# Optimization experiments

Measured on AMD Instinct MI355X. Metric: run time of the kernel, lower is better.

The kernel has to match this reference:

```python
import jax, jax.numpy as jnp
import numpy as np

N_SITES, NODE_F = 50000, 64
N_PERM, N_NEIGH = 12, 8
IN_F = N_NEIGH * NODE_F  # 512
OUT_F = 64
LN2 = float(np.log(2.0))


def setup_inputs() -> dict:
    key = jax.random.key(0)
    k1, k2, k3, k4 = jax.random.split(key, 4)
    X_sites = jax.random.normal(k1, (N_SITES, NODE_F), dtype=jnp.float32)
    X_NSs = jax.random.randint(k2, (N_SITES, N_PERM, N_NEIGH), 0, N_SITES)
    # nn.Linear(IN_F, OUT_F): weight (OUT_F, IN_F), bias (OUT_F,)
    bound = 1.0 / np.sqrt(IN_F)
    W = jax.random.uniform(k3, (OUT_F, IN_F), minval=-bound, maxval=bound, dtype=jnp.float32)
    b = jax.random.uniform(k4, (OUT_F,), minval=-bound, maxval=bound, dtype=jnp.float32)
    return {"X_sites": X_sites, "X_NSs": X_NSs, "W": W, "b": b}


def reference(X_sites, X_NSs, W, b):
    # Gather neighbor features: (N, P, K, F) -> (N, P, K*F)
    gathered = X_sites[X_NSs].reshape(X_NSs.shape[0], N_PERM, IN_F)
    # Linear: (N, P, IN_F) @ (IN_F, OUT_F) + b
    x1 = jnp.einsum('npi,oi->npo', gathered, W) + b
    # Shifted softplus: softplus(x) - log(2)  (dropout treated as identity / eval mode)
    x2 = jax.nn.softplus(x1) - LN2
    # Sum over permutations -> (N, OUT_F)
    return x2.sum(axis=1)
```

## Files before the change

kernel.cpp:

```cpp
#include <hip/hip_runtime.h>
#include <hip/hip_bf16.h>

#define N_SITES 50000
#define N_PERM  12
#define N_NEIGH 8
#define NODE_F  64
#define IN_F    512
#define OUT_F   64
#define N_TILES (N_SITES / 16)
#define LN2F    0.69314718055994530942f

#define XCHUNKS (N_SITES * NODE_F / 8)
#define WCHUNKS (OUT_F * IN_F / 8)
#define SLOT_E  520
#define BUF_E   (16 * SLOT_E)

typedef __bf16 bf16x8 __attribute__((ext_vector_type(8)));
typedef float  f32x4  __attribute__((ext_vector_type(4)));

__device__ __forceinline__ unsigned short f32_to_bf16_rne(unsigned int u) {
    u += 0x7FFFu + ((u >> 16) & 1u);
    return (unsigned short)(u >> 16);
}

__device__ __forceinline__ int probe_is_bf16(const void* Xorig) {
    int lane = threadIdx.x & 63;
    unsigned short h = ((const unsigned short*)Xorig)[2 * lane];
    int e = (h >> 7) & 0xFF;
    unsigned long long mm = __ballot(e >= 110 && e <= 140);
    return (__popcll(mm) >= 48) ? 1 : 0;
}

__device__ __forceinline__ void pack8(const uint4* src, uint4* dst, int c) {
    uint4 a = src[2 * c], b = src[2 * c + 1];
    uint4 o;
    o.x = (unsigned int)f32_to_bf16_rne(a.x) | ((unsigned int)f32_to_bf16_rne(a.y) << 16);
    o.y = (unsigned int)f32_to_bf16_rne(a.z) | ((unsigned int)f32_to_bf16_rne(a.w) << 16);
    o.z = (unsigned int)f32_to_bf16_rne(b.x) | ((unsigned int)f32_to_bf16_rne(b.y) << 16);
    o.w = (unsigned int)f32_to_bf16_rne(b.z) | ((unsigned int)f32_to_bf16_rne(b.w) << 16);
    dst[c] = o;
}

__global__ void convert_all(const void* __restrict__ Xv, const void* __restrict__ Wv,
                            const void* __restrict__ Bv, uint4* __restrict__ Xb,
                            uint4* __restrict__ Wb, float* __restrict__ Bf) {
    const int isbf = probe_is_bf16(Xv);
    int c = blockIdx.x * blockDim.x + threadIdx.x;
    if (c < XCHUNKS) {
        if (isbf) Xb[c] = ((const uint4*)Xv)[c];
        else      pack8((const uint4*)Xv, Xb, c);
    } else if (c < XCHUNKS + WCHUNKS) {
        int cw = c - XCHUNKS;
        if (isbf) Wb[cw] = ((const uint4*)Wv)[cw];
        else      pack8((const uint4*)Wv, Wb, cw);
    } else if (c < XCHUNKS + WCHUNKS + OUT_F) {
        int i = c - XCHUNKS - WCHUNKS;
        Bf[i] = isbf ? (float)((const __bf16*)Bv)[i] : ((const float*)Bv)[i];
    }
}

__device__ __forceinline__ float softplus_sh(float x) {
    float t = __expf(-fabsf(x));
    return fmaxf(x, 0.f) + 0.69314718056f * __log2f(1.f + t);
}

__device__ __forceinline__ void async16(const __bf16* g, __bf16* l) {
    __builtin_amdgcn_global_load_lds(
        (const __attribute__((address_space(1))) unsigned int*)g,
        (__attribute__((address_space(3))) unsigned int*)l, 16, 0, 0);
}

__global__ __launch_bounds__(256, 2)
void lcnn_dma(const void* __restrict__ Xorig, const __bf16* __restrict__ Xb,
              const int* __restrict__ NS, const __bf16* __restrict__ Wb,
              const float* __restrict__ Bf, void* __restrict__ outv)
{
    __shared__ __align__(16) __bf16 Abuf[2][BUF_E];

    const int wave = threadIdx.x >> 6;
    const int lane = threadIdx.x & 63;
    const int m    = lane & 15;
    const int quad = lane >> 4;
    const int mk   = m & 7;
    const int mh   = m >> 3;
    const int tile = blockIdx.x;

    bf16x8 Wfrag[16];
    #pragma unroll
    for (int ks = 0; ks < 16; ++ks)
        Wfrag[ks] = *(const bf16x8*)(Wb + (size_t)(wave * 16 + m) * IN_F + ks * 32 + quad * 8);

    const float bias = Bf[wave * 16 + m];

    auto load_idx = [&](int p_, int out[4]) {
        #pragma unroll
        for (int i = 0; i < 4; ++i) {
            int t = wave * 4 + i;
            int s = ((t & 1) << 3) + (lane >> 3);
            int k = t >> 1;
            out[i] = NS[(size_t)(tile * 16 + s) * (N_PERM * N_NEIGH) + p_ * N_NEIGH + k];
        }
    };
    auto stage = [&](int buf_, const int idxv[4]) {
        const int csrc = (lane & 7) ^ (lane >> 3);
        #pragma unroll
        for (int i = 0; i < 4; ++i) {
            int t = wave * 4 + i;
            async16(Xb + (size_t)idxv[i] * NODE_F + csrc * 8, &Abuf[buf_][t * SLOT_E]);
        }
    };

    int idxn[4];
    load_idx(0, idxn);
    stage(0, idxn);
    load_idx(1, idxn);
    __syncthreads();

    f32x4 sum = {0.f, 0.f, 0.f, 0.f};
    for (int p = 0; p < N_PERM; ++p) {
        if (p < N_PERM - 1) stage((p + 1) & 1, idxn);
        if (p < N_PERM - 2) load_idx(p + 2, idxn);

        f32x4 acc = {0.f, 0.f, 0.f, 0.f};
        const __bf16* bb = &Abuf[p & 1][0];
        #pragma unroll
        for (int ks = 0; ks < 16; ++ks) {
            int t_r = (ks >> 1) * 2 + mh;
            int j   = ((ks & 1) << 2) | quad;
            bf16x8 afr = *(const bf16x8*)(bb + t_r * SLOT_E + mk * 64 + ((j ^ mk) << 3));
            acc = __builtin_amdgcn_mfma_f32_16x16x32_bf16(afr, Wfrag[ks], acc, 0, 0, 0);
        }
        #pragma unroll
        for (int r = 0; r < 4; ++r) sum[r] += softplus_sh(acc[r] + bias);
        __syncthreads();
    }

    const int isbf = probe_is_bf16(Xorig);
    #pragma unroll
    for (int r = 0; r < 4; ++r) {
        size_t pos = (size_t)(tile * 16 + quad * 4 + r) * OUT_F + wave * 16 + m;
        float v = sum[r] - 12.0f * LN2F;
        if (isbf) ((__bf16*)outv)[pos] = (__bf16)v;
        else      ((float*)outv)[pos]  = v;
    }
}

__global__ void lcnn_fallback(const float* __restrict__ X, const int* __restrict__ NS,
                              const float* __restrict__ W, const float* __restrict__ B,
                              float* __restrict__ out) {
    int t = blockIdx.x * blockDim.x + threadIdx.x;
    if (t >= N_SITES * OUT_F) return;
    int sitei = t >> 6, o = t & 63;
    const int* ns = NS + (size_t)sitei * 96;
    float s = 0.f;
    for (int p = 0; p < N_PERM; ++p) {
        float x = B[o];
        for (int n = 0; n < N_NEIGH; ++n) {
            const float* xr = X + (size_t)ns[p * 8 + n] * NODE_F;
            const float* wr = W + (size_t)o * IN_F + n * NODE_F;
            for (int f = 0; f < NODE_F; ++f) x += xr[f] * wr[f];
        }
        s += softplus_sh(x);
    }
    out[t] = s - 12.0f * LN2F;
}

extern "C" void kernel_launch(void* const* d_in, const int* in_sizes, int n_in,
                              void* d_out, int out_size, void* d_ws, size_t ws_size,
                              hipStream_t stream) {
    const void* X  = d_in[0];
    const int*  NS = (const int*)d_in[1];
    const void* W  = d_in[2];
    const void* B  = d_in[3];

    char* ws = (char*)d_ws;
    __bf16* Xb = (__bf16*)ws;
    __bf16* Wb = (__bf16*)(ws + (size_t)XCHUNKS * 16);
    float*  Bf = (float*)(ws + (size_t)(XCHUNKS + WCHUNKS) * 16);
    const bool conv = ws_size >= (size_t)(XCHUNKS + WCHUNKS) * 16 + OUT_F * 4;

    if (conv) {
        int nch = XCHUNKS + WCHUNKS + OUT_F;
        hipLaunchKernelGGL(convert_all, dim3((nch + 255) / 256), dim3(256), 0, stream,
                           X, W, B, (uint4*)Xb, (uint4*)Wb, Bf);
        hipLaunchKernelGGL(lcnn_dma, dim3(N_TILES), dim3(256), 0, stream,
                           X, Xb, NS, Wb, Bf, d_out);
    } else {
        hipLaunchKernelGGL(lcnn_fallback,
                           dim3((N_SITES * OUT_F + 255) / 256), dim3(256), 0, stream,
                           (const float*)X, NS, (const float*)W, (const float*)B,
                           (float*)d_out);
    }
}
```

Measured before the change: 146.1 us.

## Use two waves per block with each wave computing two 16-column output fragments

Blocks shrink from four waves to two. Each wave now holds W fragments for 32 output columns and issues two MFMAs per A fragment read from LDS. This halves LDS A-fragment reads per MFMA and doubles each wave's share of gather staging. In exchange it doubles W register usage, to 128 VGPRs for the fragments, and each wave issues twice as many async gathers, which could hurt latency hiding or occupancy.

```diff
diff --git a/kernel.cpp b/kernel.cpp
--- a/kernel.cpp
+++ b/kernel.cpp
@@ -70,14 +70,14 @@
         (__attribute__((address_space(3))) unsigned int*)l, 16, 0, 0);
 }
 
-__global__ __launch_bounds__(256, 2)
+__global__ __launch_bounds__(128, 2)
 void lcnn_dma(const void* __restrict__ Xorig, const __bf16* __restrict__ Xb,
               const int* __restrict__ NS, const __bf16* __restrict__ Wb,
               const float* __restrict__ Bf, void* __restrict__ outv)
 {
     __shared__ __align__(16) __bf16 Abuf[2][BUF_E];
 
-    const int wave = threadIdx.x >> 6;
+    const int wn   = threadIdx.x >> 6;
     const int lane = threadIdx.x & 63;
     const int m    = lane & 15;
     const int quad = lane >> 4;
@@ -85,63 +85,80 @@
     const int mh   = m >> 3;
     const int tile = blockIdx.x;
 
-    bf16x8 Wfrag[16];
+    bf16x8 Wfrag[16][2];
     #pragma unroll
-    for (int ks = 0; ks < 16; ++ks)
-        Wfrag[ks] = *(const bf16x8*)(Wb + (size_t)(wave * 16 + m) * IN_F + ks * 32 + quad * 8);
-
-    const float bias = Bf[wave * 16 + m];
-
-    auto load_idx = [&](int p_, int out[4]) {
-        #pragma unroll
-        for (int i = 0; i < 4; ++i) {
-            int t = wave * 4 + i;
+    for (int ks = 0; ks < 16; ++ks) {
+        #pragma unroll
+        for (int nf = 0; nf < 2; ++nf)
+            Wfrag[ks][nf] = *(const bf16x8*)(Wb + (size_t)(wn * 32 + nf * 16 + m) * IN_F
+                                             + ks * 32 + quad * 8);
+    }
+
+    const float bias0 = Bf[wn * 32 + m];
+    const float bias1 = Bf[wn * 32 + 16 + m];
+
+    auto load_idx = [&](int p_, int out[8]) {
+        #pragma unroll
+        for (int i = 0; i < 8; ++i) {
+            int t = wn * 8 + i;
             int s = ((t & 1) << 3) + (lane >> 3);
             int k = t >> 1;
             out[i] = NS[(size_t)(tile * 16 + s) * (N_PERM * N_NEIGH) + p_ * N_NEIGH + k];
         }
     };
-    auto stage = [&](int buf_, const int idxv[4]) {
+    auto stage = [&](int buf_, const int idxv[8]) {
         const int csrc = (lane & 7) ^ (lane >> 3);
         #pragma unroll
-        for (int i = 0; i < 4; ++i) {
-            int t = wave * 4 + i;
+        for (int i = 0; i < 8; ++i) {
+            int t = wn * 8 + i;
             async16(Xb + (size_t)idxv[i] * NODE_F + csrc * 8, &Abuf[buf_][t * SLOT_E]);
         }
     };
 
-    int idxn[4];
+    int idxn[8];
     load_idx(0, idxn);
     stage(0, idxn);
     load_idx(1, idxn);
     __syncthreads();
 
-    f32x4 sum = {0.f, 0.f, 0.f, 0.f};
+    f32x4 sum0 = {0.f, 0.f, 0.f, 0.f};
+    f32x4 sum1 = {0.f, 0.f, 0.f, 0.f};
     for (int p = 0; p < N_PERM; ++p) {
         if (p < N_PERM - 1) stage((p + 1) & 1, idxn);
         if (p < N_PERM - 2) load_idx(p + 2, idxn);
 
-        f32x4 acc = {0.f, 0.f, 0.f, 0.f};
+        f32x4 acc0 = {0.f, 0.f, 0.f, 0.f};
+        f32x4 acc1 = {0.f, 0.f, 0.f, 0.f};
         const __bf16* bb = &Abuf[p & 1][0];
         #pragma unroll
         for (int ks = 0; ks < 16; ++ks) {
             int t_r = (ks >> 1) * 2 + mh;
             int j   = ((ks & 1) << 2) | quad;
             bf16x8 afr = *(const bf16x8*)(bb + t_r * SLOT_E + mk * 64 + ((j ^ mk) << 3));
-            acc = __builtin_amdgcn_mfma_f32_16x16x32_bf16(afr, Wfrag[ks], acc, 0, 0, 0);
-        }
-        #pragma unroll
-        for (int r = 0; r < 4; ++r) sum[r] += softplus_sh(acc[r] + bias);
+            acc0 = __builtin_amdgcn_mfma_f32_16x16x32_bf16(afr, Wfrag[ks][0], acc0, 0, 0, 0);
+            acc1 = __builtin_amdgcn_mfma_f32_16x16x32_bf16(afr, Wfrag[ks][1], acc1, 0, 0, 0);
+        }
+        #pragma unroll
+        for (int r = 0; r < 4; ++r) {
+            sum0[r] += softplus_sh(acc0[r] + bias0);
+            sum1[r] += softplus_sh(acc1[r] + bias1);
+        }
         __syncthreads();
     }
 
     const int isbf = probe_is_bf16(Xorig);
     #pragma unroll
     for (int r = 0; r < 4; ++r) {
-        size_t pos = (size_t)(tile * 16 + quad * 4 + r) * OUT_F + wave * 16 + m;
-        float v = sum[r] - 12.0f * LN2F;
-        if (isbf) ((__bf16*)outv)[pos] = (__bf16)v;
-        else      ((float*)outv)[pos]  = v;
+        size_t pos = (size_t)(tile * 16 + quad * 4 + r) * OUT_F + wn * 32 + m;
+        float v0 = sum0[r] - 12.0f * LN2F;
+        float v1 = sum1[r] - 12.0f * LN2F;
+        if (isbf) {
+            ((__bf16*)outv)[pos]      = (__bf16)v0;
+            ((__bf16*)outv)[pos + 16] = (__bf16)v1;
+        } else {
+            ((float*)outv)[pos]      = v0;
+            ((float*)outv)[pos + 16] = v1;
+        }
     }
 }
 
@@ -183,7 +200,7 @@
         int nch = XCHUNKS + WCHUNKS + OUT_F;
         hipLaunchKernelGGL(convert_all, dim3((nch + 255) / 256), dim3(256), 0, stream,
                            X, W, B, (uint4*)Xb, (uint4*)Wb, Bf);
-        hipLaunchKernelGGL(lcnn_dma, dim3(N_TILES), dim3(256), 0, stream,
+        hipLaunchKernelGGL(lcnn_dma, dim3(N_TILES), dim3(128), 0, stream,
                            X, Xb, NS, Wb, Bf, d_out);
     } else {
         hipLaunchKernelGGL(lcnn_fallback,
```

Result: slower. 156.0 us (+6.8%).

## Stage gathered rows through registers with a deeper prefetch pipeline

Applied to the files above, without the earlier changes.

Replaces the direct global-to-LDS async loads with plain global loads into registers, which are written to LDS one iteration later. Indices are now loaded three permutations ahead and rows two ahead. The permutation loop is fully unrolled and the final barrier is skipped. Occupancy is raised to three blocks per CU, trading extra registers and LDS store instructions for more latency hiding of the gather.

```diff
diff --git a/kernel.cpp b/kernel.cpp
--- a/kernel.cpp
+++ b/kernel.cpp
@@ -64,13 +64,7 @@
     return fmaxf(x, 0.f) + 0.69314718056f * __log2f(1.f + t);
 }
 
-__device__ __forceinline__ void async16(const __bf16* g, __bf16* l) {
-    __builtin_amdgcn_global_load_lds(
-        (const __attribute__((address_space(1))) unsigned int*)g,
-        (__attribute__((address_space(3))) unsigned int*)l, 16, 0, 0);
-}
-
-__global__ __launch_bounds__(256, 2)
+__global__ __launch_bounds__(256, 3)
 void lcnn_dma(const void* __restrict__ Xorig, const __bf16* __restrict__ Xb,
               const int* __restrict__ NS, const __bf16* __restrict__ Wb,
               const float* __restrict__ Bf, void* __restrict__ outv)
@@ -101,25 +95,40 @@
             out[i] = NS[(size_t)(tile * 16 + s) * (N_PERM * N_NEIGH) + p_ * N_NEIGH + k];
         }
     };
-    auto stage = [&](int buf_, const int idxv[4]) {
-        const int csrc = (lane & 7) ^ (lane >> 3);
+    const int csrc = (lane & 7) ^ (lane >> 3);
+    auto glo = [&](uint4 G[4], const int idxv[4]) {
+        #pragma unroll
+        for (int i = 0; i < 4; ++i)
+            G[i] = *(const uint4*)(Xb + (size_t)idxv[i] * NODE_F + csrc * 8);
+    };
+    auto stage_write = [&](int buf_, const uint4 G[4]) {
         #pragma unroll
         for (int i = 0; i < 4; ++i) {
             int t = wave * 4 + i;
-            async16(Xb + (size_t)idxv[i] * NODE_F + csrc * 8, &Abuf[buf_][t * SLOT_E]);
+            *(uint4*)(&Abuf[buf_][t * SLOT_E + (size_t)lane * 8]) = G[i];
         }
     };
 
-    int idxn[4];
-    load_idx(0, idxn);
-    stage(0, idxn);
-    load_idx(1, idxn);
+    uint4 GA[4], GB[4];
+    int idxA[4], idxB[4];
+
+    load_idx(0, idxA);
+    glo(GA, idxA);
+    load_idx(1, idxB);
+    stage_write(0, GA);
+    glo(GB, idxB);
+    load_idx(2, idxA);
     __syncthreads();
 
     f32x4 sum = {0.f, 0.f, 0.f, 0.f};
+    #pragma unroll
     for (int p = 0; p < N_PERM; ++p) {
-        if (p < N_PERM - 1) stage((p + 1) & 1, idxn);
-        if (p < N_PERM - 2) load_idx(p + 2, idxn);
+        if (p < N_PERM - 2) { if (p & 1) glo(GB, idxB); else glo(GA, idxA); }
+        if (p < N_PERM - 1) {
+            if (p & 1) stage_write((p + 1) & 1, GA);
+            else       stage_write((p + 1) & 1, GB);
+        }
+        if (p < N_PERM - 3) { if (p & 1) load_idx(p + 3, idxA); else load_idx(p + 3, idxB); }
 
         f32x4 acc = {0.f, 0.f, 0.f, 0.f};
         const __bf16* bb = &Abuf[p & 1][0];
@@ -132,7 +141,7 @@
         }
         #pragma unroll
         for (int r = 0; r < 4; ++r) sum[r] += softplus_sh(acc[r] + bias);
-        __syncthreads();
+        if (p < N_PERM - 1) __syncthreads();
     }
 
     const int isbf = probe_is_bf16(Xorig);
```

New measurement: 352.1 us. 2.41x slower.

## Replace async global-to-LDS loads with register-staged two-deep gather pipeline

Applied to the files above, without the earlier changes.

Drops the global_load_lds direct-to-LDS path. Gathered neighbor rows are now loaded into registers two permutations ahead and written to the LDS double buffer one step ahead, and index loads are prefetched three steps ahead. The permutation loop is fully unrolled, the final barrier is skipped, and launch bounds are raised to ask for three blocks per SM. This adds register pressure from the eight uint4 staging registers and adds explicit LDS store instructions in return for deeper latency hiding and higher occupancy.

```diff
diff --git a/kernel.cpp b/kernel.cpp
--- a/kernel.cpp
+++ b/kernel.cpp
@@ -64,13 +64,7 @@
     return fmaxf(x, 0.f) + 0.69314718056f * __log2f(1.f + t);
 }
 
-__device__ __forceinline__ void async16(const __bf16* g, __bf16* l) {
-    __builtin_amdgcn_global_load_lds(
-        (const __attribute__((address_space(1))) unsigned int*)g,
-        (__attribute__((address_space(3))) unsigned int*)l, 16, 0, 0);
-}
-
-__global__ __launch_bounds__(256, 2)
+__global__ __launch_bounds__(256, 3)
 void lcnn_dma(const void* __restrict__ Xorig, const __bf16* __restrict__ Xb,
               const int* __restrict__ NS, const __bf16* __restrict__ Wb,
               const float* __restrict__ Bf, void* __restrict__ outv)
@@ -92,34 +86,56 @@
 
     const float bias = Bf[wave * 16 + m];
 
-    auto load_idx = [&](int p_, int out[4]) {
-        #pragma unroll
-        for (int i = 0; i < 4; ++i) {
-            int t = wave * 4 + i;
-            int s = ((t & 1) << 3) + (lane >> 3);
-            int k = t >> 1;
-            out[i] = NS[(size_t)(tile * 16 + s) * (N_PERM * N_NEIGH) + p_ * N_NEIGH + k];
-        }
-    };
-    auto stage = [&](int buf_, const int idxv[4]) {
-        const int csrc = (lane & 7) ^ (lane >> 3);
-        #pragma unroll
-        for (int i = 0; i < 4; ++i) {
-            int t = wave * 4 + i;
-            async16(Xb + (size_t)idxv[i] * NODE_F + csrc * 8, &Abuf[buf_][t * SLOT_E]);
-        }
-    };
-
-    int idxn[4];
-    load_idx(0, idxn);
-    stage(0, idxn);
-    load_idx(1, idxn);
+    const int srow = lane >> 3;
+    const int csrc = (lane & 7) ^ srow;
+    const int* ns0 = NS + (size_t)(tile * 16 + srow)     * (N_PERM * N_NEIGH) + wave * 2;
+    const int* ns1 = NS + (size_t)(tile * 16 + srow + 8) * (N_PERM * N_NEIGH) + wave * 2;
+
+#define LIDX(iv, p_) do {                                                     \
+        (iv).x = ns0[(p_) * N_NEIGH];     (iv).y = ns1[(p_) * N_NEIGH];       \
+        (iv).z = ns0[(p_) * N_NEIGH + 1]; (iv).w = ns1[(p_) * N_NEIGH + 1];   \
+    } while (0)
+
+#define GLO(g0, g1, g2, g3, iv) do {                                          \
+        g0 = *(const uint4*)(Xb + (size_t)(iv).x * NODE_F + csrc * 8);        \
+        g1 = *(const uint4*)(Xb + (size_t)(iv).y * NODE_F + csrc * 8);        \
+        g2 = *(const uint4*)(Xb + (size_t)(iv).z * NODE_F + csrc * 8);        \
+        g3 = *(const uint4*)(Xb + (size_t)(iv).w * NODE_F + csrc * 8);        \
+    } while (0)
+
+#define STW(buf_, g0, g1, g2, g3) do {                                        \
+        *(uint4*)(&Abuf[buf_][(wave * 4 + 0) * SLOT_E + lane * 8]) = g0;      \
+        *(uint4*)(&Abuf[buf_][(wave * 4 + 1) * SLOT_E + lane * 8]) = g1;      \
+        *(uint4*)(&Abuf[buf_][(wave * 4 + 2) * SLOT_E + lane * 8]) = g2;      \
+        *(uint4*)(&Abuf[buf_][(wave * 4 + 3) * SLOT_E + lane * 8]) = g3;      \
+    } while (0)
+
+    uint4 A0, A1, A2, A3, B0, B1, B2, B3;
+    int4  iA, iB;
+
+    LIDX(iA, 0);
+    GLO(A0, A1, A2, A3, iA);
+    LIDX(iB, 1);
+    STW(0, A0, A1, A2, A3);
+    GLO(B0, B1, B2, B3, iB);
+    LIDX(iA, 2);
     __syncthreads();
 
     f32x4 sum = {0.f, 0.f, 0.f, 0.f};
+    #pragma unroll
     for (int p = 0; p < N_PERM; ++p) {
-        if (p < N_PERM - 1) stage((p + 1) & 1, idxn);
-        if (p < N_PERM - 2) load_idx(p + 2, idxn);
+        if (p < N_PERM - 2) {
+            if (p & 1) GLO(B0, B1, B2, B3, iB);
+            else       GLO(A0, A1, A2, A3, iA);
+        }
+        if (p < N_PERM - 1) {
+            if (p & 1) STW((p + 1) & 1, A0, A1, A2, A3);
+            else       STW((p + 1) & 1, B0, B1, B2, B3);
+        }
+        if (p < N_PERM - 3) {
+            if (p & 1) LIDX(iA, p + 3);
+            else       LIDX(iB, p + 3);
+        }
 
         f32x4 acc = {0.f, 0.f, 0.f, 0.f};
         const __bf16* bb = &Abuf[p & 1][0];
@@ -132,8 +148,12 @@
         }
         #pragma unroll
         for (int r = 0; r < 4; ++r) sum[r] += softplus_sh(acc[r] + bias);
-        __syncthreads();
-    }
+        if (p < N_PERM - 1) __syncthreads();
+    }
+
+#undef LIDX
+#undef GLO
+#undef STW
 
     const int isbf = probe_is_bf16(Xorig);
     #pragma unroll
```

Measured after the change: 158.1 us. 8.2% more time.
